# Optimization experiments

Measured on AMD Instinct MI355X. Metric: run time of the kernel, lower is better.

The kernel has to match this reference:

```python
import jax, jax.numpy as jnp
import numpy as np

H = 1024
B, S = 8, 2048


def setup_inputs() -> dict:
    key = jax.random.key(0)
    ks = jax.random.split(key, 9)
    scale = 1.0 / np.sqrt(H)
    x = jax.random.normal(ks[0], (B, S, H), dtype=jnp.float32)
    attention_mask = jnp.ones((B, S), dtype=jnp.int32)
    wq = jax.random.uniform(ks[1], (H, H), jnp.float32, -scale, scale)
    bq = jax.random.uniform(ks[2], (H,), jnp.float32, -scale, scale)
    wk = jax.random.uniform(ks[3], (H, H), jnp.float32, -scale, scale)
    bk = jax.random.uniform(ks[4], (H,), jnp.float32, -scale, scale)
    wv = jax.random.uniform(ks[5], (H, H), jnp.float32, -scale, scale)
    bv = jax.random.uniform(ks[6], (H,), jnp.float32, -scale, scale)
    wo = jax.random.uniform(ks[7], (H, H), jnp.float32, -scale, scale)
    bo = jax.random.uniform(ks[8], (H,), jnp.float32, -scale, scale)
    return {"x": x, "attention_mask": attention_mask,
            "wq": wq, "bq": bq, "wk": wk, "bk": bk,
            "wv": wv, "bv": bv, "wo": wo, "bo": bo}


def reference(x, attention_mask, wq, bq, wk, bk, wv, bv, wo, bo):
    # x: [B, S, H]; attention_mask: [B, S] (1 = keep key, 0 = pad)
    hidden_dim = x.shape[-1]
    seq = x.shape[1]
    Q = jnp.einsum('bsh,dh->bsd', x, wq) + bq
    K = jnp.einsum('bsh,dh->bsd', x, wk) + bk
    V = jnp.einsum('bsh,dh->bsd', x, wv) + bv
    # scores: [B, S, S], scaled by 1/sqrt(hidden_dim) as in the original
    scores = jnp.einsum('bqd,bkd->bqk', Q, K) / jnp.sqrt(
        jnp.asarray(hidden_dim, dtype=x.dtype))
    causal = jnp.triu(jnp.ones((seq, seq), dtype=bool), k=1)  # [S, S]
    pad = ~(attention_mask.astype(bool))[:, None, :]          # [B, 1, S]
    mask = causal[None, :, :] | pad                           # [B, S, S]
    scores = jnp.where(mask, -jnp.inf, scores)
    probs = jax.nn.softmax(scores, axis=-1)
    # dropout_rate = 0.0 -> identity
    out = jnp.einsum('bqk,bkd->bqd', probs, V)
    out = jnp.einsum('bsd,hd->bsh', out, wo) + bo
    return out
```

## Files before the change

kernel.cpp:

```cpp
#include <hip/hip_runtime.h>
#include <hip/hip_bf16.h>


typedef __bf16 bf16x8 __attribute__((ext_vector_type(8)));
typedef float f32x4 __attribute__((ext_vector_type(4)));

static constexpr int HD = 1024;
static constexpr int BB = 8;
static constexpr int SS = 2048;
static constexpr long long SH = (long long)SS * HD;

__device__ __forceinline__ unsigned short f2bf(float f) {
  unsigned u = __builtin_bit_cast(unsigned, f);
  return (unsigned short)((u + 0x7FFFu + ((u >> 16) & 1u)) >> 16);
}
__device__ __forceinline__ f32x4 mfma16(bf16x8 a, bf16x8 b, f32x4 c) {
  return __builtin_amdgcn_mfma_f32_16x16x32_bf16(a, b, c, 0, 0, 0);
}
__device__ __forceinline__ void gload_lds16(const void* g, void* l) {
  __builtin_amdgcn_global_load_lds(
      (const __attribute__((address_space(1))) void*)g,
      (__attribute__((address_space(3))) void*)l, 16, 0, 0);
}

#define WAIT_LGKM0() do { asm volatile("s_waitcnt lgkmcnt(0)" ::: "memory"); \
  __builtin_amdgcn_sched_barrier(0); } while (0)
#define WAIT_VM(n) do { asm volatile("s_waitcnt vmcnt(" #n ")" ::: "memory"); \
  __builtin_amdgcn_sched_barrier(0); } while (0)

__device__ __forceinline__ bf16x8 rf(const unsigned short* tile, int row,
                                     int colb) {
  const int byte = row * 64 + (colb ^ (((row >> 1) & 3) << 4));
  return *reinterpret_cast<const bf16x8*>(
      reinterpret_cast<const char*>(tile) + byte);
}

struct TC {
  int wid, wm, wn, cb, rr, ccl, l16;
  const unsigned short *pA, *pA2, *pB;
};

__device__ __forceinline__ TC tc_make(const unsigned short* A,
                                      const unsigned short* B, int m0, int n0,
                                      long long lda, long long ldb) {
  TC t;
  const int tid = threadIdx.x;
  t.wid = tid >> 6;
  const int lane = tid & 63;
  t.wm = t.wid >> 1;
  t.wn = t.wid & 1;
  t.l16 = lane & 15;
  t.cb = (lane >> 4) * 16;
  t.rr = (lane >> 4) * 4;
  t.ccl = t.l16;
  const int rowt = tid >> 2;
  const int colg = (((tid & 3) ^ ((rowt >> 1) & 3)) * 8);
  t.pA = A + (long long)(m0 + rowt) * lda + colg;
  t.pA2 = t.pA + 128 * lda;
  t.pB = B + (long long)(n0 + rowt) * ldb + colg;
  return t;
}

#define STAGE(Abuf, Bbuf, kt) do { \
  gload_lds16(t.pA + (kt), (Abuf) + t.wid * 512); \
  gload_lds16(t.pA2 + (kt), (Abuf) + 4096 + t.wid * 512); \
  gload_lds16(t.pB + (kt), (Bbuf) + t.wid * 512); \
} while (0)

__device__ __forceinline__ void run_tile(
    const TC& t, int NK, unsigned short* As0, unsigned short* As1,
    unsigned short* Bs0, unsigned short* Bs1, f32x4 (&acc)[4][4]) {
  STAGE(As0, Bs0, 0);
  STAGE(As1, Bs1, 32);
  WAIT_VM(3);
  __builtin_amdgcn_s_barrier();
  for (int k = 0; k < NK; ++k) {
    const unsigned short* A = (k & 1) ? As1 : As0;
    const unsigned short* B = (k & 1) ? Bs1 : Bs0;
    bf16x8 af[4], bf[4];
#pragma unroll
    for (int i = 0; i < 4; ++i)
      af[i] = rf(A, t.wm * 64 + i * 16 + t.l16, t.cb);
#pragma unroll
    for (int i = 0; i < 4; ++i)
      bf[i] = rf(B, t.wn * 64 + i * 16 + t.l16, t.cb);
    WAIT_LGKM0();
    __builtin_amdgcn_s_barrier();
    if (k + 2 < NK) {
      unsigned short* An = (k & 1) ? As1 : As0;
      unsigned short* Bn = (k & 1) ? Bs1 : Bs0;
      STAGE(An, Bn, (long long)(k + 2) * 32);
    }
    __builtin_amdgcn_s_setprio(1);
#pragma unroll
    for (int mi = 0; mi < 4; ++mi)
#pragma unroll
      for (int ni = 0; ni < 4; ++ni)
        acc[mi][ni] = mfma16(af[mi], bf[ni], acc[mi][ni]);
    __builtin_amdgcn_s_setprio(0);
    if (k + 2 < NK) { WAIT_VM(3); } else { WAIT_VM(0); }
    __builtin_amdgcn_s_barrier();
  }
}

#define SHARED_TILES() \
  __shared__ __align__(16) unsigned short As0[8192], As1[8192]; \
  __shared__ __align__(16) unsigned short Bs0[4096], Bs1[4096]

__global__ __launch_bounds__(512, 4) void qkv_kernel(
    const unsigned short* __restrict__ X, const unsigned short* __restrict__ W,
    const float* __restrict__ bq, const float* __restrict__ bk,
    const float* __restrict__ bv, unsigned short* __restrict__ Q,
    unsigned short* __restrict__ K, unsigned short* __restrict__ Vt) {
  SHARED_TILES();
  const int lin = blockIdx.x;
  const int swz = (lin & 7) * 192 + (lin >> 3);
  const int m0 = (swz / 24) * 256, n0 = (swz % 24) * 128;
  TC t = tc_make(X, W, m0, n0, HD, HD);
  f32x4 acc[4][4] = {};
  run_tile(t, 32, As0, As1, Bs0, Bs1, acc);
#pragma unroll
  for (int mi = 0; mi < 4; ++mi)
#pragma unroll
    for (int ni = 0; ni < 4; ++ni) {
      const int gn = n0 + t.wn * 64 + ni * 16 + t.ccl;
      float bias;
      if (gn < 1024) bias = bq[gn];
      else if (gn < 2048) bias = bk[gn - 1024];
      else bias = bv[gn - 2048];
#pragma unroll
      for (int j = 0; j < 4; ++j) {
        const int gm = m0 + t.wm * 64 + mi * 16 + t.rr + j;
        const unsigned short v = f2bf(acc[mi][ni][j] + bias);
        if (gn < 1024) {
          Q[(long long)gm * HD + gn] = v;
        } else if (gn < 2048) {
          K[(long long)gm * HD + (gn - 1024)] = v;
        } else {
          const int b = gm >> 11, s = gm & 2047, d = gn - 2048;
          Vt[b * SH + (long long)d * SS + s] = v;
        }
      }
    }
}

__global__ __launch_bounds__(512, 4) void scores_kernel(
    const unsigned short* __restrict__ Q, const unsigned short* __restrict__ Km,
    const int* __restrict__ mask, unsigned short* __restrict__ S,
    float* __restrict__ rowsum) {
  SHARED_TILES();
  __shared__ float rsl[512];
  const int lin = blockIdx.x;
  const long long b = lin & 7;
  int tt = lin >> 3;
  int mt = 0, cum = 0;
  while (tt >= cum + 2 * mt + 2) { cum += 2 * mt + 2; ++mt; }
  const int nt = tt - cum;
  const int m0 = mt * 256, n0 = nt * 128;
  TC t = tc_make(Q + b * SH, Km + b * SH, m0, n0, HD, HD);
  f32x4 acc[4][4] = {};
  run_tile(t, 32, As0, As1, Bs0, Bs1, acc);

  unsigned short* Sb = S + b * (long long)SS * SS;
  const int* mb = mask + b * SS;
  float* rs = rowsum + b * SS;
#pragma unroll
  for (int mi = 0; mi < 4; ++mi)
#pragma unroll
    for (int j = 0; j < 4; ++j) {
      const int lrow = t.wm * 64 + mi * 16 + t.rr + j;
      const int gm = m0 + lrow;
      float rsum = 0.0f;
#pragma unroll
      for (int ni = 0; ni < 4; ++ni) {
        const int gn = n0 + t.wn * 64 + ni * 16 + t.ccl;
        const bool dead = (gn > gm) || (mb[gn] == 0);
        const float pv = dead ? 0.0f : __expf(acc[mi][ni][j] * 0.03125f);
        Sb[(long long)gm * SS + gn] = f2bf(pv);
        rsum += pv;
      }
#pragma unroll
      for (int o = 1; o < 16; o <<= 1) rsum += __shfl_xor(rsum, o);
      if (t.ccl == 0) rsl[t.wn * 256 + lrow] = rsum;
    }
  __syncthreads();
  const int tid = threadIdx.x;
  if (tid < 256) atomicAdd(&rs[m0 + tid], rsl[tid] + rsl[256 + tid]);
}

__global__ __launch_bounds__(512, 4) void pv_kernel(
    const unsigned short* __restrict__ S, const unsigned short* __restrict__ Vt,
    const float* __restrict__ rowsum, unsigned short* __restrict__ AO) {
  SHARED_TILES();
  const int lin = blockIdx.x;
  const long long b = lin & 7;
  const int r = lin >> 3;
  const int jp = r >> 1, par = r & 1;
  const int nt = jp >> 2;
  const int q = jp & 3;
  const int mt = par ? 7 - q : q;
  const int m0 = mt * 256, n0 = nt * 128;
  const int NK = 8 * (mt + 1);
  TC t = tc_make(S + b * (long long)SS * SS, Vt + b * SH, m0, n0, SS, SS);
  f32x4 acc[4][4] = {};
  run_tile(t, NK, As0, As1, Bs0, Bs1, acc);
  const float* rs = rowsum + b * SS;
#pragma unroll
  for (int mi = 0; mi < 4; ++mi)
#pragma unroll
    for (int j = 0; j < 4; ++j) {
      const int gm = m0 + t.wm * 64 + mi * 16 + t.rr + j;
      const float inv = 1.0f / rs[gm];
#pragma unroll
      for (int ni = 0; ni < 4; ++ni) {
        const int gn = n0 + t.wn * 64 + ni * 16 + t.ccl;
        AO[(b * SS + gm) * (long long)HD + gn] = f2bf(acc[mi][ni][j] * inv);
      }
    }
}

__global__ __launch_bounds__(512, 4) void oproj_kernel(
    const unsigned short* __restrict__ AO, const unsigned short* __restrict__ W,
    const float* __restrict__ bo, float* __restrict__ out) {
  SHARED_TILES();
  const int lin = blockIdx.x;
  const int swz = (lin & 7) * 64 + (lin >> 3);
  const int m0 = (swz >> 3) * 256, n0 = (swz & 7) * 128;
  TC t = tc_make(AO, W, m0, n0, HD, HD);
  f32x4 acc[4][4] = {};
  run_tile(t, 32, As0, As1, Bs0, Bs1, acc);
#pragma unroll
  for (int mi = 0; mi < 4; ++mi)
#pragma unroll
    for (int ni = 0; ni < 4; ++ni) {
      const int gn = n0 + t.wn * 64 + ni * 16 + t.ccl;
      const float bias = bo[gn];
#pragma unroll
      for (int j = 0; j < 4; ++j) {
        const int gm = m0 + t.wm * 64 + mi * 16 + t.rr + j;
        out[(long long)gm * HD + gn] = acc[mi][ni][j] + bias;
      }
    }
}

__global__ __launch_bounds__(256) void cast_all(
    const float* __restrict__ x, const float* __restrict__ wq,
    const float* __restrict__ wk, const float* __restrict__ wv,
    const float* __restrict__ wo, unsigned short* __restrict__ xb,
    unsigned short* __restrict__ wqkvb, unsigned short* __restrict__ wob,
    float* __restrict__ rowsum) {
  const int NX4 = (int)((long long)BB * SS * HD / 4);
  const int W4 = HD * HD / 4;
  const int RS4 = BB * SS / 4;
  const int TOT = NX4 + 4 * W4 + RS4;
  int idx = blockIdx.x * blockDim.x + threadIdx.x;
  const int stride = gridDim.x * blockDim.x;
  for (int u = idx; u < TOT; u += stride) {
    if (u >= NX4 + 4 * W4) {
      *reinterpret_cast<float4*>(rowsum + (u - NX4 - 4 * W4) * 4) =
          make_float4(0.f, 0.f, 0.f, 0.f);
      continue;
    }
    const float* src;
    unsigned short* dst;
    int off;
    if (u < NX4) {
      src = x; dst = xb; off = u;
    } else {
      const int v = u - NX4;
      const int seg = v >> 18;
      off = v & (W4 - 1);
      if (seg == 0) { src = wq; dst = wqkvb; }
      else if (seg == 1) { src = wk; dst = wqkvb + HD * HD; }
      else if (seg == 2) { src = wv; dst = wqkvb + 2 * HD * HD; }
      else { src = wo; dst = wob; }
    }
    float4 f = *reinterpret_cast<const float4*>(src + off * 4);
    ushort4 o;
    o.x = f2bf(f.x); o.y = f2bf(f.y); o.z = f2bf(f.z); o.w = f2bf(f.w);
    *reinterpret_cast<ushort4*>(dst + off * 4) = o;
  }
}

extern "C" void kernel_launch(void* const* d_in, const int* in_sizes, int n_in,
                              void* d_out, int out_size, void* d_ws, size_t ws_size,
                              hipStream_t stream) {
  const float* x = (const float*)d_in[0];
  const int* amask = (const int*)d_in[1];
  const float* wq = (const float*)d_in[2];
  const float* bq = (const float*)d_in[3];
  const float* wk = (const float*)d_in[4];
  const float* bk = (const float*)d_in[5];
  const float* wv = (const float*)d_in[6];
  const float* bv = (const float*)d_in[7];
  const float* wo = (const float*)d_in[8];
  const float* bo = (const float*)d_in[9];
  float* out = (float*)d_out;

  const long long NX = (long long)BB * SS * HD;
  char* p = (char*)d_ws;
  unsigned short* xb = (unsigned short*)p;     p += NX * 2;
  unsigned short* wqkvb = (unsigned short*)p;  p += 3LL * HD * HD * 2;
  unsigned short* wob = (unsigned short*)p;    p += (long long)HD * HD * 2;
  unsigned short* Qb = (unsigned short*)p;     p += NX * 2;
  unsigned short* Kb = (unsigned short*)p;     p += NX * 2;
  unsigned short* Vtb = (unsigned short*)p;    p += NX * 2;
  unsigned short* Sb = (unsigned short*)p;     p += (long long)BB * SS * SS * 2;
  float* rowsum = (float*)p;                   p += (long long)BB * SS * 4;
  unsigned short* AOb = xb;

  cast_all<<<dim3(2048), 256, 0, stream>>>(x, wq, wk, wv, wo, xb, wqkvb, wob,
                                           rowsum);

  qkv_kernel<<<dim3(1536), 512, 0, stream>>>(xb, wqkvb, bq, bk, bv, Qb, Kb,
                                             Vtb);

  scores_kernel<<<dim3(576), 512, 0, stream>>>(Qb, Kb, amask, Sb, rowsum);
  pv_kernel<<<dim3(512), 512, 0, stream>>>(Sb, Vtb, rowsum, AOb);

  oproj_kernel<<<dim3(512), 512, 0, stream>>>(AOb, wob, bo, out);
}
```

Baseline: 348.1 us.

## Triple-buffer LDS tiles to drop one barrier per k-step

The shared GEMM mainloop moves from double to triple LDS buffering with rotating read, next and write pointers. The prefetch for step k+2 now goes into a third buffer, so the barrier between reading fragments and issuing the prefetch is gone. This costs 72 KB of LDS per block instead of 48 KB, which may lower the number of resident blocks per CU in all four GEMM kernels.

After: 338.7 us. 2.7% less time.

```diff
diff --git a/kernel.cpp b/kernel.cpp
--- a/kernel.cpp
+++ b/kernel.cpp
@@ -68,29 +68,26 @@
 } while (0)
 
 __device__ __forceinline__ void run_tile(
-    const TC& t, int NK, unsigned short* As0, unsigned short* As1,
-    unsigned short* Bs0, unsigned short* Bs1, f32x4 (&acc)[4][4]) {
-  STAGE(As0, Bs0, 0);
-  STAGE(As1, Bs1, 32);
+    const TC& t, int NK, unsigned short* A0, unsigned short* A1,
+    unsigned short* A2, unsigned short* B0, unsigned short* B1,
+    unsigned short* B2, f32x4 (&acc)[4][4]) {
+  STAGE(A0, B0, 0);
+  STAGE(A1, B1, 32);
   WAIT_VM(3);
   __builtin_amdgcn_s_barrier();
+  unsigned short *Ar = A0, *Br = B0;
+  unsigned short *An = A1, *Bn = B1;
+  unsigned short *Aw = A2, *Bw = B2;
   for (int k = 0; k < NK; ++k) {
-    const unsigned short* A = (k & 1) ? As1 : As0;
-    const unsigned short* B = (k & 1) ? Bs1 : Bs0;
     bf16x8 af[4], bf[4];
 #pragma unroll
     for (int i = 0; i < 4; ++i)
-      af[i] = rf(A, t.wm * 64 + i * 16 + t.l16, t.cb);
+      af[i] = rf(Ar, t.wm * 64 + i * 16 + t.l16, t.cb);
 #pragma unroll
     for (int i = 0; i < 4; ++i)
-      bf[i] = rf(B, t.wn * 64 + i * 16 + t.l16, t.cb);
+      bf[i] = rf(Br, t.wn * 64 + i * 16 + t.l16, t.cb);
     WAIT_LGKM0();
-    __builtin_amdgcn_s_barrier();
-    if (k + 2 < NK) {
-      unsigned short* An = (k & 1) ? As1 : As0;
-      unsigned short* Bn = (k & 1) ? Bs1 : Bs0;
-      STAGE(An, Bn, (long long)(k + 2) * 32);
-    }
+    if (k + 2 < NK) STAGE(Aw, Bw, (long long)(k + 2) * 32);
     __builtin_amdgcn_s_setprio(1);
 #pragma unroll
     for (int mi = 0; mi < 4; ++mi)
@@ -98,14 +95,18 @@
       for (int ni = 0; ni < 4; ++ni)
         acc[mi][ni] = mfma16(af[mi], bf[ni], acc[mi][ni]);
     __builtin_amdgcn_s_setprio(0);
-    if (k + 2 < NK) { WAIT_VM(3); } else { WAIT_VM(0); }
-    __builtin_amdgcn_s_barrier();
+    if (k + 1 < NK) {
+      if (k + 2 < NK) { WAIT_VM(3); } else { WAIT_VM(0); }
+      __builtin_amdgcn_s_barrier();
+      unsigned short* ta = Ar; Ar = An; An = Aw; Aw = ta;
+      unsigned short* tb = Br; Br = Bn; Bn = Bw; Bw = tb;
+    }
   }
 }
 
 #define SHARED_TILES() \
-  __shared__ __align__(16) unsigned short As0[8192], As1[8192]; \
-  __shared__ __align__(16) unsigned short Bs0[4096], Bs1[4096]
+  __shared__ __align__(16) unsigned short As0[8192], As1[8192], As2[8192]; \
+  __shared__ __align__(16) unsigned short Bs0[4096], Bs1[4096], Bs2[4096]
 
 __global__ __launch_bounds__(512, 4) void qkv_kernel(
     const unsigned short* __restrict__ X, const unsigned short* __restrict__ W,
@@ -118,7 +119,7 @@
   const int m0 = (swz / 24) * 256, n0 = (swz % 24) * 128;
   TC t = tc_make(X, W, m0, n0, HD, HD);
   f32x4 acc[4][4] = {};
-  run_tile(t, 32, As0, As1, Bs0, Bs1, acc);
+  run_tile(t, 32, As0, As1, As2, Bs0, Bs1, Bs2, acc);
 #pragma unroll
   for (int mi = 0; mi < 4; ++mi)
 #pragma unroll
@@ -159,7 +160,7 @@
   const int m0 = mt * 256, n0 = nt * 128;
   TC t = tc_make(Q + b * SH, Km + b * SH, m0, n0, HD, HD);
   f32x4 acc[4][4] = {};
-  run_tile(t, 32, As0, As1, Bs0, Bs1, acc);
+  run_tile(t, 32, As0, As1, As2, Bs0, Bs1, Bs2, acc);
 
   unsigned short* Sb = S + b * (long long)SS * SS;
   const int* mb = mask + b * SS;
@@ -203,7 +204,7 @@
   const int NK = 8 * (mt + 1);
   TC t = tc_make(S + b * (long long)SS * SS, Vt + b * SH, m0, n0, SS, SS);
   f32x4 acc[4][4] = {};
-  run_tile(t, NK, As0, As1, Bs0, Bs1, acc);
+  run_tile(t, NK, As0, As1, As2, Bs0, Bs1, Bs2, acc);
   const float* rs = rowsum + b * SS;
 #pragma unroll
   for (int mi = 0; mi < 4; ++mi)
@@ -228,7 +229,7 @@
   const int m0 = (swz >> 3) * 256, n0 = (swz & 7) * 128;
   TC t = tc_make(AO, W, m0, n0, HD, HD);
   f32x4 acc[4][4] = {};
-  run_tile(t, 32, As0, As1, Bs0, Bs1, acc);
+  run_tile(t, 32, As0, As1, As2, Bs0, Bs1, Bs2, acc);
 #pragma unroll
   for (int mi = 0; mi < 4; ++mi)
 #pragma unroll
```
